# Optimization experiments

Measured on AMD Instinct MI355X. Metric: run time of the kernel, lower is better.

Reference implementation:

```python
import jax, jax.numpy as jnp
import numpy as np

# --- fan-beam (flat detector) FBP geometry constants, matching init geo dict ---
V, U = 720, 736            # sino_views, nDetecU
NX = NY = 512              # nVoxelX, nVoxelY
SVOX = 400.0               # sVoxelX = sVoxelY (mm)
DU = 1.2858                # dDetecU (mm)
DSO, DOD = 595.0, 490.6    # source-origin, origin-detector distances
DSD = DSO + DOD
DBETA = 2.0 * np.pi / V    # angular step (full 2*pi scan, endpoint=False)


def _ramp_filter_fft():
    """Ram-Lak ramp filter (Kak & Slaney discrete spatial kernel), FFT'd for fast conv."""
    n = np.arange(-(U - 1), U)
    h = np.zeros(2 * U - 1, np.float64)
    h[U - 1] = 1.0 / (4.0 * DU * DU)
    odd = (np.abs(n) % 2 == 1)
    h[odd] = -1.0 / (np.pi * n[odd] * DU) ** 2
    L = int(2 ** np.ceil(np.log2(2 * (2 * U - 1))))  # zero-pad length (linear conv)
    return jnp.asarray(np.fft.fft(h, L).astype(np.complex64)), L

_HF, _L = _ramp_filter_fft()


def setup_inputs() -> dict:
    key = jax.random.key(0)
    sinogram = jax.random.uniform(key, (1, 1, V, U), dtype=jnp.float32)
    return {"sinogram": sinogram}


def reference(sinogram):
    # --- 1) cosine weighting of each detector sample ---
    sino = sinogram.reshape(V, U)
    us = (jnp.arange(U, dtype=jnp.float32) - (U - 1) / 2.0) * DU  # detector coords
    sino_w = sino * (DSD / jnp.sqrt(DSD * DSD + us * us))

    # --- 2) Ram-Lak ramp filtering per view (FFT linear convolution) ---
    Qf = jnp.fft.ifft(jnp.fft.fft(sino_w, n=_L, axis=1) * _HF[None, :], axis=1)
    Q = (jnp.real(Qf)[:, U - 1:2 * U - 1] * DU).astype(jnp.float32)  # [V, U]

    # --- 3) weighted fan-beam backprojection (scan over angles, O(Nx*Ny) carry) ---
    dx = SVOX / NX
    xs = (jnp.arange(NX, dtype=jnp.float32) - (NX - 1) / 2.0) * dx
    X, Y = jnp.meshgrid(xs, xs, indexing='ij')  # [NX, NY]
    betas = jnp.linspace(0.0, 2.0 * np.pi, V, endpoint=False).astype(jnp.float32)

    def body(img, ang_q):
        beta, q = ang_q                       # q: filtered projection [U]
        cb, sb = jnp.cos(beta), jnp.sin(beta)
        t = X * cb + Y * sb                   # coord along detector direction
        s = -X * sb + Y * cb                  # coord toward source
        D = DSO - s                           # source-to-pixel axial distance
        u = DSD * t / D                       # flat-detector intersection (mm)
        idx = u / DU + (U - 1) / 2.0          # fractional detector index
        i0 = jnp.clip(jnp.floor(idx), 0, U - 2).astype(jnp.int32)
        f = idx - i0
        val = q[i0] * (1.0 - f) + q[i0 + 1] * f
        val = jnp.where((idx >= 0.0) & (idx <= U - 1.0), val, 0.0)
        return img + (DSO / D) ** 2 * val, None

    img0 = jnp.zeros((NX, NY), jnp.float32)
    img, _ = jax.lax.scan(body, img0, (betas, Q))
    # 0.5 factor: full 2*pi fan scan covers each ray twice
    return (img * (0.5 * DBETA)).reshape(1, 1, NX, NY)
```

## Files before the change

### kernel.cpp

```cpp
#include <hip/hip_runtime.h>
#include <math.h>

#define NV 720
#define NU 736
#define NUP 768
#define NXY 512
#define NM 368

__global__ __launch_bounds__(368) void prep_kernel(const float* __restrict__ sino,
                                                   float* __restrict__ swI,
                                                   float4* __restrict__ trig,
                                                   float* __restrict__ out_zero) {
    const int v = blockIdx.x;
    const int m = threadIdx.x;
    const int vb = v >> 2, vv = v & 3;
    const float DSD2 = (float)(1085.6 * 1085.6);
    #pragma unroll
    for (int pu = 0; pu < 2; ++pu) {
        const int u = 2 * m + pu;
        float us = ((float)u - 367.5f) * 1.2858f;
        float cw = 1085.6f / sqrtf(DSD2 + us * us);
        swI[((size_t)vb * NM + m) * 8 + pu * 4 + vv] = sino[v * NU + u] * cw;
    }
    if (m == 0) {
        float beta = (float)((double)v * (2.0 * M_PI / 720.0));
        float cb = cosf(beta), sb = sinf(beta);
        const float K = (float)(1085.6 / 1.2858);
        trig[v] = make_float4(cb * K, sb * K, cb, sb);
    }
    for (int i = v * 368 + m; i < NXY * NXY; i += 720 * 368)
        out_zero[i] = 0.0f;
}

__global__ __launch_bounds__(512) void filter_kernel(const float* __restrict__ swI,
                                                     float* __restrict__ Q) {
    __shared__ float wco[736];
    __shared__ float part[3][8][96];
    const int bx = blockIdx.x;
    const int q = bx & 3;
    const int vb = bx >> 2;
    const int v0 = vb * 4;
    const int tid = threadIdx.x;
    const int J0 = tid & 127;

    for (int i = tid; i < 736; i += 512) {
        double n = (double)(2 * i - 735);
        double a = M_PI * n * 1.2858;
        wco[i] = (float)(-1.0 / (a * a));
    }
    __syncthreads();

    const int m0 = __builtin_amdgcn_readfirstlane(92 * (tid >> 7));
    const int tz = m0 / 92;
    const float* sw = swI + (size_t)vb * NM * 8;
    const float* sp = sw + (size_t)m0 * 8;

    float a00 = 0.f, a01 = 0.f, a02 = 0.f, a03 = 0.f;
    float a10 = 0.f, a11 = 0.f, a12 = 0.f, a13 = 0.f;
    const int J0c = min(J0, 91);
    const int y0 = J0c + 367 + 92 * q;
    const float* wp = &wco[y0 - m0];

    #pragma unroll 4
    for (int mm = 0; mm < 92; ++mm) {
        const float w0 = wp[-mm];
        const float w1 = wp[1 - mm];
        const float* s = sp + mm * 8;
        const float s10 = s[4], s11 = s[5], s12 = s[6], s13 = s[7];
        const float s00 = s[0], s01 = s[1], s02 = s[2], s03 = s[3];
        a00 = fmaf(w0, s10, a00); a01 = fmaf(w0, s11, a01);
        a02 = fmaf(w0, s12, a02); a03 = fmaf(w0, s13, a03);
        a10 = fmaf(w1, s00, a10); a11 = fmaf(w1, s01, a11);
        a12 = fmaf(w1, s02, a12); a13 = fmaf(w1, s03, a13);
    }

    if (tz != 0 && J0 < 92) {
        part[tz - 1][0][J0] = a00; part[tz - 1][1][J0] = a01;
        part[tz - 1][2][J0] = a02; part[tz - 1][3][J0] = a03;
        part[tz - 1][4][J0] = a10; part[tz - 1][5][J0] = a11;
        part[tz - 1][6][J0] = a12; part[tz - 1][7][J0] = a13;
    }
    __syncthreads();

    if (tz == 0 && J0 < 92) {
        #pragma unroll
        for (int g = 0; g < 3; ++g) {
            a00 += part[g][0][J0]; a01 += part[g][1][J0];
            a02 += part[g][2][J0]; a03 += part[g][3][J0];
            a10 += part[g][4][J0]; a11 += part[g][5][J0];
            a12 += part[g][6][J0]; a13 += part[g][7][J0];
        }
        const float H0 = (float)(1.0 / (4.0 * 1.2858 * 1.2858));
        const int mc = J0 + 92 * q;
        const float4 c0 = *(const float4*)(sw + (size_t)mc * 8);
        const float4 c1 = *(const float4*)(sw + (size_t)mc * 8 + 4);
        a00 = fmaf(H0, c0.x, a00); a01 = fmaf(H0, c0.y, a01);
        a02 = fmaf(H0, c0.z, a02); a03 = fmaf(H0, c0.w, a03);
        a10 = fmaf(H0, c1.x, a10); a11 = fmaf(H0, c1.y, a11);
        a12 = fmaf(H0, c1.z, a12); a13 = fmaf(H0, c1.w, a13);
        const int j0i = 2 * (J0 + 92 * q);
        const float DU = 1.2858f;
        *(float2*)&Q[(v0 + 0) * NUP + j0i] = make_float2(a00 * DU, a10 * DU);
        *(float2*)&Q[(v0 + 1) * NUP + j0i] = make_float2(a01 * DU, a11 * DU);
        *(float2*)&Q[(v0 + 2) * NUP + j0i] = make_float2(a02 * DU, a12 * DU);
        *(float2*)&Q[(v0 + 3) * NUP + j0i] = make_float2(a03 * DU, a13 * DU);
    }
}

__global__ __launch_bounds__(256) void bp_kernel(const float* __restrict__ Q,
                                                 const float4* __restrict__ trig,
                                                 float* __restrict__ out) {
    __shared__ float win[2][4][NUP];
    const int b = blockIdx.x;
    const int c = b & 15;
    const int blk = b >> 4;
    const int bx = blk >> 4;
    const int by = blk & 15;
    const int t = threadIdx.x;
    const int w = t >> 6;
    const int l = t & 63;
    const int iq = (bx << 4) + ((w >> 1) << 3) + (l >> 3);
    const int jq = (by << 4) + ((w & 1) << 3) + (l & 7);

    const float dx = 400.0f / 512.0f;
    const float X = ((float)iq - 255.5f) * dx;
    const float Y = ((float)jq - 255.5f) * dx;
    const float Kc = (float)(1085.6 / 1.2858);

    float acc0 = 0.0f, acc1 = 0.0f, acc2 = 0.0f, acc3 = 0.0f;
    const bool inr = fmaf(X, X, Y * Y) <= 236.5f * 236.5f;
    const bool myint = __all(inr);

    const int nk = (c < 4) ? 12 : 11;
    const float* rowp = Q + (size_t)(c + 180 * w) * NUP;
    const float4* tvp = trig + c;

    #pragma unroll
    for (int ch = 0; ch < 3; ++ch)
        __builtin_amdgcn_global_load_lds(
            (const __attribute__((address_space(1))) void*)(rowp + ch * 256 + l * 4),
            (__attribute__((address_space(3))) void*)&win[0][w][ch * 256],
            16, 0, 0);

    for (int it = 0; it < nk; ++it) {
        __syncthreads();
        if (it + 1 < nk) {
            const float* rn = rowp + 16 * NUP;
            #pragma unroll
            for (int ch = 0; ch < 3; ++ch)
                __builtin_amdgcn_global_load_lds(
                    (const __attribute__((address_space(1))) void*)(rn + ch * 256 + l * 4),
                    (__attribute__((address_space(3))) void*)&win[(it + 1) & 1][w][ch * 256],
                    16, 0, 0);
        }
        const float* winf = &win[it & 1][0][0];

        if (myint) {
            const float4 tv = tvp[0];
            float a = fmaf(tv.z, X, tv.w * Y);
            float bb = fmaf(tv.z, Y, -tv.w * X);
            float aK = a * Kc, bK = bb * Kc;
            float D0 = 595.0f - bb, D1 = 595.0f + a, D2 = 595.0f + bb, D3 = 595.0f - a;
            float r0 = __builtin_amdgcn_rcpf(D0);
            float r1 = __builtin_amdgcn_rcpf(D1);
            float r2 = __builtin_amdgcn_rcpf(D2);
            float r3 = __builtin_amdgcn_rcpf(D3);
            float fi0 = fmaf(aK,  r0, 367.5f);
            float fi1 = fmaf(bK,  r1, 367.5f);
            float fi2 = fmaf(-aK, r2, 367.5f);
            float fi3 = fmaf(-bK, r3, 367.5f);
            int im[4] = {(int)fi0, (int)fi1, (int)fi2, (int)fi3};
            float ff[4] = {__builtin_amdgcn_fractf(fi0), __builtin_amdgcn_fractf(fi1),
                           __builtin_amdgcn_fractf(fi2), __builtin_amdgcn_fractf(fi3)};
            float gg[4] = {r0 * r0, r1 * r1, r2 * r2, r3 * r3};
            float* accp[4] = {&acc0, &acc1, &acc2, &acc3};
            #pragma unroll
            for (int m = 0; m < 4; ++m) {
                #pragma unroll
                for (int k = 0; k < 4; ++k) {
                    const float* p = winf + (k * NUP + im[m]);
                    float q0 = p[0];
                    float q1 = p[1];
                    float val = fmaf(ff[m], q1 - q0, q0);
                    *accp[(m - k) & 3] = fmaf(gg[m], val, *accp[(m - k) & 3]);
                }
            }
        } else {
            const float4 tvs[4] = {tvp[0], tvp[180], tvp[360], tvp[540]};
            const float pX[4] = {X, Y, -X, -Y};
            const float pY[4] = {Y, -X, -Y, X};
            float* accp[4] = {&acc0, &acc1, &acc2, &acc3};
            #pragma unroll
            for (int j = 0; j < 4; ++j) {
                float Xm = pX[j], Ym = pY[j];
                #pragma unroll
                for (int k = 0; k < 4; ++k) {
                    const float4 tv = tvs[k];
                    float t2 = fmaf(tv.x, Xm, tv.y * Ym);
                    float D  = fmaf(tv.w, Xm, fmaf(tv.z, -Ym, 595.0f));
                    float rD = __builtin_amdgcn_rcpf(D);
                    float fidx = fmaf(t2, rD, 367.5f);
                    int i0c = min(max((int)fidx, 0), NU - 2);
                    float f = __builtin_amdgcn_fractf(fidx);
                    const float* p = winf + (k * NUP + i0c);
                    float q0 = p[0];
                    float q1 = p[1];
                    float val = fmaf(f, q1 - q0, q0);
                    float cen = fidx - 367.5f;
                    float g = (__builtin_fabsf(cen) <= 367.5f) ? rD * rD : 0.0f;
                    *accp[j] = fmaf(g, val, *accp[j]);
                }
            }
        }
        rowp += 16 * NUP;
        tvp += 16;
    }
    const float SC = (float)(595.0 * 595.0 * 0.5 * (2.0 * M_PI / 720.0));
    const int ir = 511 - iq, jr = 511 - jq;
    unsafeAtomicAdd(&out[iq * NXY + jq], acc0 * SC);
    unsafeAtomicAdd(&out[jq * NXY + ir], acc1 * SC);
    unsafeAtomicAdd(&out[ir * NXY + jr], acc2 * SC);
    unsafeAtomicAdd(&out[jr * NXY + iq], acc3 * SC);
}

extern "C" void kernel_launch(void* const* d_in, const int* in_sizes, int n_in,
                              void* d_out, int out_size, void* d_ws, size_t ws_size,
                              hipStream_t stream) {
    const float* sino = (const float*)d_in[0];
    float* out = (float*)d_out;
    float* Q = (float*)d_ws;
    float4* trig = (float4*)((char*)d_ws + (size_t)NV * NUP * sizeof(float));
    float* swI = (float*)((char*)trig + (size_t)NV * sizeof(float4));

    prep_kernel<<<720, 368, 0, stream>>>(sino, swI, trig, out);
    filter_kernel<<<720, 512, 0, stream>>>(swI, Q);
    bp_kernel<<<4096, 256, 0, stream>>>(Q, trig, out);
}
```

Measured before the change: 117.5 us.

## Fuse prep, filter and backprojection into one persistent kernel with grid barriers

Replaces the three kernel launches with a single persistent kernel of 1024 blocks that synchronises phases through atomic-counter grid barriers. Cosine weighting now happens inside the filter phase in shared memory, so the swI intermediate and its global round trip go away. The backprojection phase loops over four pixel tiles per block instead of launching 4096 blocks. This removes launch gaps and one intermediate buffer, but adds a hipMemset launch and grid-barrier spin cost. It also assumes all 1024 blocks are co-resident; the barrier has a timeout that could silently break correctness if they are not.

```diff
diff --git a/kernel.cpp b/kernel.cpp
--- a/kernel.cpp
+++ b/kernel.cpp
@@ -5,222 +5,234 @@
 #define NU 736
 #define NUP 768
 #define NXY 512
-#define NM 368
-
-__global__ __launch_bounds__(368) void prep_kernel(const float* __restrict__ sino,
-                                                   float* __restrict__ swI,
-                                                   float4* __restrict__ trig,
-                                                   float* __restrict__ out_zero) {
-    const int v = blockIdx.x;
-    const int m = threadIdx.x;
-    const int vb = v >> 2, vv = v & 3;
-    const float DSD2 = (float)(1085.6 * 1085.6);
-    #pragma unroll
-    for (int pu = 0; pu < 2; ++pu) {
-        const int u = 2 * m + pu;
-        float us = ((float)u - 367.5f) * 1.2858f;
-        float cw = 1085.6f / sqrtf(DSD2 + us * us);
-        swI[((size_t)vb * NM + m) * 8 + pu * 4 + vv] = sino[v * NU + u] * cw;
-    }
-    if (m == 0) {
-        float beta = (float)((double)v * (2.0 * M_PI / 720.0));
+#define GRID 1024
+
+__device__ __forceinline__ void gsync(int* bar, int slot, int tid) {
+    __syncthreads();
+    if (tid == 0) {
+        __threadfence_system();
+        int* cnt = bar + 2 * slot;
+        int* flag = bar + 2 * slot + 1;
+        if (__hip_atomic_fetch_add(cnt, 1, __ATOMIC_ACQ_REL, __HIP_MEMORY_SCOPE_AGENT)
+            == GRID - 1) {
+            __hip_atomic_store(flag, 1, __ATOMIC_RELEASE, __HIP_MEMORY_SCOPE_AGENT);
+        } else {
+            long long t0 = clock64();
+            while (__hip_atomic_load(flag, __ATOMIC_ACQUIRE, __HIP_MEMORY_SCOPE_AGENT) == 0) {
+                __builtin_amdgcn_s_sleep(8);
+                if (clock64() - t0 > 100000000LL) break;
+            }
+        }
+        __threadfence_system();
+    }
+    __syncthreads();
+}
+
+__global__ __launch_bounds__(256, 4) void fused_kernel(const float* __restrict__ sino,
+                                                       float* __restrict__ Q,
+                                                       float4* __restrict__ trig,
+                                                       float* __restrict__ out,
+                                                       int* __restrict__ bar) {
+    __shared__ __align__(16) char smem[24576];
+    const int bid = blockIdx.x;
+    const int tid = threadIdx.x;
+    const int gid = bid * 256 + tid;
+
+    out[gid] = 0.0f;
+    if (gid < NV) {
+        float beta = (float)((double)gid * (2.0 * M_PI / 720.0));
         float cb = cosf(beta), sb = sinf(beta);
         const float K = (float)(1085.6 / 1.2858);
-        trig[v] = make_float4(cb * K, sb * K, cb, sb);
-    }
-    for (int i = v * 368 + m; i < NXY * NXY; i += 720 * 368)
-        out_zero[i] = 0.0f;
-}
-
-__global__ __launch_bounds__(512) void filter_kernel(const float* __restrict__ swI,
-                                                     float* __restrict__ Q) {
-    __shared__ float wco[736];
-    __shared__ float part[3][8][96];
-    const int bx = blockIdx.x;
-    const int q = bx & 3;
-    const int vb = bx >> 2;
-    const int v0 = vb * 4;
-    const int tid = threadIdx.x;
-    const int J0 = tid & 127;
-
-    for (int i = tid; i < 736; i += 512) {
-        double n = (double)(2 * i - 735);
-        double a = M_PI * n * 1.2858;
-        wco[i] = (float)(-1.0 / (a * a));
-    }
-    __syncthreads();
-
-    const int m0 = __builtin_amdgcn_readfirstlane(92 * (tid >> 7));
-    const int tz = m0 / 92;
-    const float* sw = swI + (size_t)vb * NM * 8;
-    const float* sp = sw + (size_t)m0 * 8;
-
-    float a00 = 0.f, a01 = 0.f, a02 = 0.f, a03 = 0.f;
-    float a10 = 0.f, a11 = 0.f, a12 = 0.f, a13 = 0.f;
-    const int J0c = min(J0, 91);
-    const int y0 = J0c + 367 + 92 * q;
-    const float* wp = &wco[y0 - m0];
-
-    #pragma unroll 4
-    for (int mm = 0; mm < 92; ++mm) {
-        const float w0 = wp[-mm];
-        const float w1 = wp[1 - mm];
-        const float* s = sp + mm * 8;
-        const float s10 = s[4], s11 = s[5], s12 = s[6], s13 = s[7];
-        const float s00 = s[0], s01 = s[1], s02 = s[2], s03 = s[3];
-        a00 = fmaf(w0, s10, a00); a01 = fmaf(w0, s11, a01);
-        a02 = fmaf(w0, s12, a02); a03 = fmaf(w0, s13, a03);
-        a10 = fmaf(w1, s00, a10); a11 = fmaf(w1, s01, a11);
-        a12 = fmaf(w1, s02, a12); a13 = fmaf(w1, s03, a13);
-    }
-
-    if (tz != 0 && J0 < 92) {
-        part[tz - 1][0][J0] = a00; part[tz - 1][1][J0] = a01;
-        part[tz - 1][2][J0] = a02; part[tz - 1][3][J0] = a03;
-        part[tz - 1][4][J0] = a10; part[tz - 1][5][J0] = a11;
-        part[tz - 1][6][J0] = a12; part[tz - 1][7][J0] = a13;
-    }
-    __syncthreads();
-
-    if (tz == 0 && J0 < 92) {
-        #pragma unroll
-        for (int g = 0; g < 3; ++g) {
-            a00 += part[g][0][J0]; a01 += part[g][1][J0];
-            a02 += part[g][2][J0]; a03 += part[g][3][J0];
-            a10 += part[g][4][J0]; a11 += part[g][5][J0];
-            a12 += part[g][6][J0]; a13 += part[g][7][J0];
-        }
-        const float H0 = (float)(1.0 / (4.0 * 1.2858 * 1.2858));
-        const int mc = J0 + 92 * q;
-        const float4 c0 = *(const float4*)(sw + (size_t)mc * 8);
-        const float4 c1 = *(const float4*)(sw + (size_t)mc * 8 + 4);
-        a00 = fmaf(H0, c0.x, a00); a01 = fmaf(H0, c0.y, a01);
-        a02 = fmaf(H0, c0.z, a02); a03 = fmaf(H0, c0.w, a03);
-        a10 = fmaf(H0, c1.x, a10); a11 = fmaf(H0, c1.y, a11);
-        a12 = fmaf(H0, c1.z, a12); a13 = fmaf(H0, c1.w, a13);
-        const int j0i = 2 * (J0 + 92 * q);
-        const float DU = 1.2858f;
-        *(float2*)&Q[(v0 + 0) * NUP + j0i] = make_float2(a00 * DU, a10 * DU);
-        *(float2*)&Q[(v0 + 1) * NUP + j0i] = make_float2(a01 * DU, a11 * DU);
-        *(float2*)&Q[(v0 + 2) * NUP + j0i] = make_float2(a02 * DU, a12 * DU);
-        *(float2*)&Q[(v0 + 3) * NUP + j0i] = make_float2(a03 * DU, a13 * DU);
-    }
-}
-
-__global__ __launch_bounds__(256) void bp_kernel(const float* __restrict__ Q,
-                                                 const float4* __restrict__ trig,
-                                                 float* __restrict__ out) {
-    __shared__ float win[2][4][NUP];
-    const int b = blockIdx.x;
-    const int c = b & 15;
-    const int blk = b >> 4;
-    const int bx = blk >> 4;
-    const int by = blk & 15;
-    const int t = threadIdx.x;
+        trig[gid] = make_float4(cb * K, sb * K, cb, sb);
+    }
+    gsync(bar, 0, tid);
+
+    if (bid < 720) {
+        float (*s4)[368][4] = (float(*)[368][4])smem;
+        float* wco = (float*)(smem + 11776);
+        float (*part)[96] = (float(*)[96])(smem + 14720);
+        const int q = bid & 3;
+        const int vb = bid >> 2;
+        const int v0 = vb * 4;
+        const int tz = tid >> 7;
+        const int J0 = tid & 127;
+
+        const float DSD2 = (float)(1085.6 * 1085.6);
+        for (int i = tid; i < 4 * NU; i += 256) {
+            const int vv = i / NU, u = i - vv * NU;
+            float us = ((float)u - 367.5f) * 1.2858f;
+            float cw = 1085.6f / sqrtf(DSD2 + us * us);
+            s4[u & 1][u >> 1][vv] = sino[(v0 + vv) * NU + u] * cw;
+        }
+        for (int i = tid; i < 736; i += 256) {
+            double n = (double)(2 * i - 735);
+            double a = M_PI * n * 1.2858;
+            wco[i] = (float)(-1.0 / (a * a));
+        }
+        __syncthreads();
+
+        const int m0 = 184 * tz;
+        float a00 = 0.f, a01 = 0.f, a02 = 0.f, a03 = 0.f;
+        float a10 = 0.f, a11 = 0.f, a12 = 0.f, a13 = 0.f;
+        const int J0c = min(J0, 91);
+        const int y0 = J0c + 367 + 92 * q;
+        const float* wp = &wco[y0 - m0];
+
+        #pragma unroll 4
+        for (int mm = 0; mm < 184; ++mm) {
+            const int m = m0 + mm;
+            const float w0 = wp[-mm];
+            const float w1 = wp[1 - mm];
+            const float4 sv1 = *(const float4*)&s4[1][m][0];
+            const float4 sv0 = *(const float4*)&s4[0][m][0];
+            a00 = fmaf(w0, sv1.x, a00); a01 = fmaf(w0, sv1.y, a01);
+            a02 = fmaf(w0, sv1.z, a02); a03 = fmaf(w0, sv1.w, a03);
+            a10 = fmaf(w1, sv0.x, a10); a11 = fmaf(w1, sv0.y, a11);
+            a12 = fmaf(w1, sv0.z, a12); a13 = fmaf(w1, sv0.w, a13);
+        }
+
+        if (tz == 1 && J0 < 92) {
+            part[0][J0] = a00; part[1][J0] = a01; part[2][J0] = a02; part[3][J0] = a03;
+            part[4][J0] = a10; part[5][J0] = a11; part[6][J0] = a12; part[7][J0] = a13;
+        }
+        __syncthreads();
+
+        if (tz == 0 && J0 < 92) {
+            a00 += part[0][J0]; a01 += part[1][J0];
+            a02 += part[2][J0]; a03 += part[3][J0];
+            a10 += part[4][J0]; a11 += part[5][J0];
+            a12 += part[6][J0]; a13 += part[7][J0];
+            const float H0 = (float)(1.0 / (4.0 * 1.2858 * 1.2858));
+            const int mc = J0 + 92 * q;
+            const float4 c0 = *(const float4*)&s4[0][mc][0];
+            const float4 c1 = *(const float4*)&s4[1][mc][0];
+            a00 = fmaf(H0, c0.x, a00); a01 = fmaf(H0, c0.y, a01);
+            a02 = fmaf(H0, c0.z, a02); a03 = fmaf(H0, c0.w, a03);
+            a10 = fmaf(H0, c1.x, a10); a11 = fmaf(H0, c1.y, a11);
+            a12 = fmaf(H0, c1.z, a12); a13 = fmaf(H0, c1.w, a13);
+            const int j0i = 2 * mc;
+            const float DU = 1.2858f;
+            *(float2*)&Q[(v0 + 0) * NUP + j0i] = make_float2(a00 * DU, a10 * DU);
+            *(float2*)&Q[(v0 + 1) * NUP + j0i] = make_float2(a01 * DU, a11 * DU);
+            *(float2*)&Q[(v0 + 2) * NUP + j0i] = make_float2(a02 * DU, a12 * DU);
+            *(float2*)&Q[(v0 + 3) * NUP + j0i] = make_float2(a03 * DU, a13 * DU);
+        }
+    }
+    gsync(bar, 1, tid);
+
+    float (*win)[4][NUP] = (float(*)[4][NUP])smem;
+    const int cc = bid & 15;
+    const int t = tid;
     const int w = t >> 6;
     const int l = t & 63;
-    const int iq = (bx << 4) + ((w >> 1) << 3) + (l >> 3);
-    const int jq = (by << 4) + ((w & 1) << 3) + (l & 7);
-
     const float dx = 400.0f / 512.0f;
-    const float X = ((float)iq - 255.5f) * dx;
-    const float Y = ((float)jq - 255.5f) * dx;
     const float Kc = (float)(1085.6 / 1.2858);
-
-    float acc0 = 0.0f, acc1 = 0.0f, acc2 = 0.0f, acc3 = 0.0f;
-    const bool inr = fmaf(X, X, Y * Y) <= 236.5f * 236.5f;
-    const bool myint = __all(inr);
-
-    const int nk = (c < 4) ? 12 : 11;
-    const float* rowp = Q + (size_t)(c + 180 * w) * NUP;
-    const float4* tvp = trig + c;
-
-    #pragma unroll
-    for (int ch = 0; ch < 3; ++ch)
-        __builtin_amdgcn_global_load_lds(
-            (const __attribute__((address_space(1))) void*)(rowp + ch * 256 + l * 4),
-            (__attribute__((address_space(3))) void*)&win[0][w][ch * 256],
-            16, 0, 0);
-
-    for (int it = 0; it < nk; ++it) {
+    const int nk = (cc < 4) ? 12 : 11;
+
+    #pragma unroll 1
+    for (int ti = 0; ti < 4; ++ti) {
+        const int blk = (bid >> 4) + ti * 64;
+        const int bx = blk >> 4;
+        const int by = blk & 15;
+        const int iq = (bx << 4) + ((w >> 1) << 3) + (l >> 3);
+        const int jq = (by << 4) + ((w & 1) << 3) + (l & 7);
+        const float X = ((float)iq - 255.5f) * dx;
+        const float Y = ((float)jq - 255.5f) * dx;
+        float acc0 = 0.0f, acc1 = 0.0f, acc2 = 0.0f, acc3 = 0.0f;
+        const bool inr = fmaf(X, X, Y * Y) <= 236.5f * 236.5f;
+        const bool myint = __all(inr);
+
+        const float* rowp = Q + (size_t)(cc + 180 * w) * NUP;
+        const float4* tvp = trig + cc;
+
         __syncthreads();
-        if (it + 1 < nk) {
-            const float* rn = rowp + 16 * NUP;
-            #pragma unroll
-            for (int ch = 0; ch < 3; ++ch)
-                __builtin_amdgcn_global_load_lds(
-                    (const __attribute__((address_space(1))) void*)(rn + ch * 256 + l * 4),
-                    (__attribute__((address_space(3))) void*)&win[(it + 1) & 1][w][ch * 256],
-                    16, 0, 0);
-        }
-        const float* winf = &win[it & 1][0][0];
-
-        if (myint) {
-            const float4 tv = tvp[0];
-            float a = fmaf(tv.z, X, tv.w * Y);
-            float bb = fmaf(tv.z, Y, -tv.w * X);
-            float aK = a * Kc, bK = bb * Kc;
-            float D0 = 595.0f - bb, D1 = 595.0f + a, D2 = 595.0f + bb, D3 = 595.0f - a;
-            float r0 = __builtin_amdgcn_rcpf(D0);
-            float r1 = __builtin_amdgcn_rcpf(D1);
-            float r2 = __builtin_amdgcn_rcpf(D2);
-            float r3 = __builtin_amdgcn_rcpf(D3);
-            float fi0 = fmaf(aK,  r0, 367.5f);
-            float fi1 = fmaf(bK,  r1, 367.5f);
-            float fi2 = fmaf(-aK, r2, 367.5f);
-            float fi3 = fmaf(-bK, r3, 367.5f);
-            int im[4] = {(int)fi0, (int)fi1, (int)fi2, (int)fi3};
-            float ff[4] = {__builtin_amdgcn_fractf(fi0), __builtin_amdgcn_fractf(fi1),
-                           __builtin_amdgcn_fractf(fi2), __builtin_amdgcn_fractf(fi3)};
-            float gg[4] = {r0 * r0, r1 * r1, r2 * r2, r3 * r3};
-            float* accp[4] = {&acc0, &acc1, &acc2, &acc3};
-            #pragma unroll
-            for (int m = 0; m < 4; ++m) {
+        #pragma unroll
+        for (int ch = 0; ch < 3; ++ch)
+            __builtin_amdgcn_global_load_lds(
+                (const __attribute__((address_space(1))) void*)(rowp + ch * 256 + l * 4),
+                (__attribute__((address_space(3))) void*)&win[0][w][ch * 256],
+                16, 0, 0);
+
+        for (int it = 0; it < nk; ++it) {
+            __syncthreads();
+            if (it + 1 < nk) {
+                const float* rn = rowp + 16 * NUP;
                 #pragma unroll
-                for (int k = 0; k < 4; ++k) {
-                    const float* p = winf + (k * NUP + im[m]);
-                    float q0 = p[0];
-                    float q1 = p[1];
-                    float val = fmaf(ff[m], q1 - q0, q0);
-                    *accp[(m - k) & 3] = fmaf(gg[m], val, *accp[(m - k) & 3]);
+                for (int ch = 0; ch < 3; ++ch)
+                    __builtin_amdgcn_global_load_lds(
+                        (const __attribute__((address_space(1))) void*)(rn + ch * 256 + l * 4),
+                        (__attribute__((address_space(3))) void*)&win[(it + 1) & 1][w][ch * 256],
+                        16, 0, 0);
+            }
+            const float* winf = &win[it & 1][0][0];
+
+            if (myint) {
+                const float4 tv = tvp[0];
+                float a = fmaf(tv.z, X, tv.w * Y);
+                float bb = fmaf(tv.z, Y, -tv.w * X);
+                float aK = a * Kc, bK = bb * Kc;
+                float D0 = 595.0f - bb, D1 = 595.0f + a, D2 = 595.0f + bb, D3 = 595.0f - a;
+                float r0 = __builtin_amdgcn_rcpf(D0);
+                float r1 = __builtin_amdgcn_rcpf(D1);
+                float r2 = __builtin_amdgcn_rcpf(D2);
+                float r3 = __builtin_amdgcn_rcpf(D3);
+                float fi0 = fmaf(aK,  r0, 367.5f);
+                float fi1 = fmaf(bK,  r1, 367.5f);
+                float fi2 = fmaf(-aK, r2, 367.5f);
+                float fi3 = fmaf(-bK, r3, 367.5f);
+                int im[4] = {(int)fi0, (int)fi1, (int)fi2, (int)fi3};
+                float ff[4] = {__builtin_amdgcn_fractf(fi0), __builtin_amdgcn_fractf(fi1),
+                               __builtin_amdgcn_fractf(fi2), __builtin_amdgcn_fractf(fi3)};
+                float gg[4] = {r0 * r0, r1 * r1, r2 * r2, r3 * r3};
+                float* accp[4] = {&acc0, &acc1, &acc2, &acc3};
+                #pragma unroll
+                for (int m = 0; m < 4; ++m) {
+                    #pragma unroll
+                    for (int k = 0; k < 4; ++k) {
+                        const float* p = winf + (k * NUP + im[m]);
+                        float q0 = p[0];
+                        float q1 = p[1];
+                        float val = fmaf(ff[m], q1 - q0, q0);
+                        *accp[(m - k) & 3] = fmaf(gg[m], val, *accp[(m - k) & 3]);
+                    }
+                }
+            } else {
+                const float4 tvs[4] = {tvp[0], tvp[180], tvp[360], tvp[540]};
+                const float pX[4] = {X, Y, -X, -Y};
+                const float pY[4] = {Y, -X, -Y, X};
+                float* accp[4] = {&acc0, &acc1, &acc2, &acc3};
+                #pragma unroll
+                for (int j = 0; j < 4; ++j) {
+                    float Xm = pX[j], Ym = pY[j];
+                    #pragma unroll
+                    for (int k = 0; k < 4; ++k) {
+                        const float4 tv = tvs[k];
+                        float t2 = fmaf(tv.x, Xm, tv.y * Ym);
+                        float D  = fmaf(tv.w, Xm, fmaf(tv.z, -Ym, 595.0f));
+                        float rD = __builtin_amdgcn_rcpf(D);
+                        float fidx = fmaf(t2, rD, 367.5f);
+                        int i0c = min(max((int)fidx, 0), NU - 2);
+                        float f = __builtin_amdgcn_fractf(fidx);
+                        const float* p = winf + (k * NUP + i0c);
+                        float q0 = p[0];
+                        float q1 = p[1];
+                        float val = fmaf(f, q1 - q0, q0);
+                        float cen = fidx - 367.5f;
+                        float g = (__builtin_fabsf(cen) <= 367.5f) ? rD * rD : 0.0f;
+                        *accp[j] = fmaf(g, val, *accp[j]);
+                    }
                 }
             }
-        } else {
-            const float4 tvs[4] = {tvp[0], tvp[180], tvp[360], tvp[540]};
-            const float pX[4] = {X, Y, -X, -Y};
-            const float pY[4] = {Y, -X, -Y, X};
-            float* accp[4] = {&acc0, &acc1, &acc2, &acc3};
-            #pragma unroll
-            for (int j = 0; j < 4; ++j) {
-                float Xm = pX[j], Ym = pY[j];
-                #pragma unroll
-                for (int k = 0; k < 4; ++k) {
-                    const float4 tv = tvs[k];
-                    float t2 = fmaf(tv.x, Xm, tv.y * Ym);
-                    float D  = fmaf(tv.w, Xm, fmaf(tv.z, -Ym, 595.0f));
-                    float rD = __builtin_amdgcn_rcpf(D);
-                    float fidx = fmaf(t2, rD, 367.5f);
-                    int i0c = min(max((int)fidx, 0), NU - 2);
-                    float f = __builtin_amdgcn_fractf(fidx);
-                    const float* p = winf + (k * NUP + i0c);
-                    float q0 = p[0];
-                    float q1 = p[1];
-                    float val = fmaf(f, q1 - q0, q0);
-                    float cen = fidx - 367.5f;
-                    float g = (__builtin_fabsf(cen) <= 367.5f) ? rD * rD : 0.0f;
-                    *accp[j] = fmaf(g, val, *accp[j]);
-                }
-            }
-        }
-        rowp += 16 * NUP;
-        tvp += 16;
-    }
-    const float SC = (float)(595.0 * 595.0 * 0.5 * (2.0 * M_PI / 720.0));
-    const int ir = 511 - iq, jr = 511 - jq;
-    unsafeAtomicAdd(&out[iq * NXY + jq], acc0 * SC);
-    unsafeAtomicAdd(&out[jq * NXY + ir], acc1 * SC);
-    unsafeAtomicAdd(&out[ir * NXY + jr], acc2 * SC);
-    unsafeAtomicAdd(&out[jr * NXY + iq], acc3 * SC);
+            rowp += 16 * NUP;
+            tvp += 16;
+        }
+        const float SC = (float)(595.0 * 595.0 * 0.5 * (2.0 * M_PI / 720.0));
+        const int ir = 511 - iq, jr = 511 - jq;
+        unsafeAtomicAdd(&out[iq * NXY + jq], acc0 * SC);
+        unsafeAtomicAdd(&out[jq * NXY + ir], acc1 * SC);
+        unsafeAtomicAdd(&out[ir * NXY + jr], acc2 * SC);
+        unsafeAtomicAdd(&out[jr * NXY + iq], acc3 * SC);
+    }
 }
 
 extern "C" void kernel_launch(void* const* d_in, const int* in_sizes, int n_in,
@@ -230,9 +242,8 @@
     float* out = (float*)d_out;
     float* Q = (float*)d_ws;
     float4* trig = (float4*)((char*)d_ws + (size_t)NV * NUP * sizeof(float));
-    float* swI = (float*)((char*)trig + (size_t)NV * sizeof(float4));
-
-    prep_kernel<<<720, 368, 0, stream>>>(sino, swI, trig, out);
-    filter_kernel<<<720, 512, 0, stream>>>(swI, Q);
-    bp_kernel<<<4096, 256, 0, stream>>>(Q, trig, out);
+    int* bar = (int*)((char*)trig + (size_t)NV * sizeof(float4));
+
+    hipMemsetAsync(bar, 0, 16, stream);
+    fused_kernel<<<GRID, 256, 0, stream>>>(sino, Q, trig, out, bar);
 }
```

Measured after the change: 351.9 us. 3x slower.

## Fuse cosine-weighting prep into filter kernel and raise backprojection wave priority

Applied to the files above, without the earlier changes.

Removes the separate prep kernel. Each filter block now cosine-weights its four views straight into an interleaved shared-memory buffer, and also zeroes the output and writes the trig table. This saves a kernel launch and a global round trip through the weighted-sinogram buffer. The cost is that each of the four blocks per view group recomputes the same weighting. Partial sums move to a float4-friendly layout, and s_setprio is raised around the backprojection compute section to favour compute waves over the loading phase.

```diff
diff --git a/kernel.cpp b/kernel.cpp
--- a/kernel.cpp
+++ b/kernel.cpp
@@ -5,44 +5,39 @@
 #define NU 736
 #define NUP 768
 #define NXY 512
-#define NM 368
-
-__global__ __launch_bounds__(368) void prep_kernel(const float* __restrict__ sino,
-                                                   float* __restrict__ swI,
-                                                   float4* __restrict__ trig,
-                                                   float* __restrict__ out_zero) {
-    const int v = blockIdx.x;
-    const int m = threadIdx.x;
-    const int vb = v >> 2, vv = v & 3;
-    const float DSD2 = (float)(1085.6 * 1085.6);
-    #pragma unroll
-    for (int pu = 0; pu < 2; ++pu) {
-        const int u = 2 * m + pu;
-        float us = ((float)u - 367.5f) * 1.2858f;
-        float cw = 1085.6f / sqrtf(DSD2 + us * us);
-        swI[((size_t)vb * NM + m) * 8 + pu * 4 + vv] = sino[v * NU + u] * cw;
-    }
-    if (m == 0) {
-        float beta = (float)((double)v * (2.0 * M_PI / 720.0));
-        float cb = cosf(beta), sb = sinf(beta);
-        const float K = (float)(1085.6 / 1.2858);
-        trig[v] = make_float4(cb * K, sb * K, cb, sb);
-    }
-    for (int i = v * 368 + m; i < NXY * NXY; i += 720 * 368)
-        out_zero[i] = 0.0f;
-}
-
-__global__ __launch_bounds__(512) void filter_kernel(const float* __restrict__ swI,
-                                                     float* __restrict__ Q) {
+
+__global__ __launch_bounds__(512) void filter_kernel(const float* __restrict__ sino,
+                                                     float* __restrict__ Q,
+                                                     float4* __restrict__ trig,
+                                                     float* __restrict__ out_zero) {
+    __shared__ float s4[2][368][4];
     __shared__ float wco[736];
-    __shared__ float part[3][8][96];
+    __shared__ float part[3][128][8];
     const int bx = blockIdx.x;
     const int q = bx & 3;
     const int vb = bx >> 2;
     const int v0 = vb * 4;
     const int tid = threadIdx.x;
+    const int tz = tid >> 7;
     const int J0 = tid & 127;
 
+    for (int i = bx * 512 + tid; i < NXY * NXY; i += 720 * 512)
+        out_zero[i] = 0.0f;
+
+    if (q == 0 && tid < 4) {
+        int v = v0 + tid;
+        float beta = (float)((double)v * (2.0 * M_PI / 720.0));
+        float cb = cosf(beta), sb = sinf(beta);
+        const float K = (float)(1085.6 / 1.2858);
+        trig[v] = make_float4(cb * K, sb * K, cb, sb);
+    }
+    const float DSD2 = (float)(1085.6 * 1085.6);
+    for (int i = tid; i < 4 * NU; i += 512) {
+        const int vv = i / NU, u = i - vv * NU;
+        float us = ((float)u - 367.5f) * 1.2858f;
+        float cw = 1085.6f / sqrtf(DSD2 + us * us);
+        s4[u & 1][u >> 1][vv] = sino[(v0 + vv) * NU + u] * cw;
+    }
     for (int i = tid; i < 736; i += 512) {
         double n = (double)(2 * i - 735);
         double a = M_PI * n * 1.2858;
@@ -50,11 +45,7 @@
     }
     __syncthreads();
 
-    const int m0 = __builtin_amdgcn_readfirstlane(92 * (tid >> 7));
-    const int tz = m0 / 92;
-    const float* sw = swI + (size_t)vb * NM * 8;
-    const float* sp = sw + (size_t)m0 * 8;
-
+    const int m0 = 92 * tz;
     float a00 = 0.f, a01 = 0.f, a02 = 0.f, a03 = 0.f;
     float a10 = 0.f, a11 = 0.f, a12 = 0.f, a13 = 0.f;
     const int J0c = min(J0, 91);
@@ -63,42 +54,40 @@
 
     #pragma unroll 4
     for (int mm = 0; mm < 92; ++mm) {
+        const int m = m0 + mm;
         const float w0 = wp[-mm];
         const float w1 = wp[1 - mm];
-        const float* s = sp + mm * 8;
-        const float s10 = s[4], s11 = s[5], s12 = s[6], s13 = s[7];
-        const float s00 = s[0], s01 = s[1], s02 = s[2], s03 = s[3];
-        a00 = fmaf(w0, s10, a00); a01 = fmaf(w0, s11, a01);
-        a02 = fmaf(w0, s12, a02); a03 = fmaf(w0, s13, a03);
-        a10 = fmaf(w1, s00, a10); a11 = fmaf(w1, s01, a11);
-        a12 = fmaf(w1, s02, a12); a13 = fmaf(w1, s03, a13);
+        const float4 sv1 = *(const float4*)&s4[1][m][0];
+        const float4 sv0 = *(const float4*)&s4[0][m][0];
+        a00 = fmaf(w0, sv1.x, a00); a01 = fmaf(w0, sv1.y, a01);
+        a02 = fmaf(w0, sv1.z, a02); a03 = fmaf(w0, sv1.w, a03);
+        a10 = fmaf(w1, sv0.x, a10); a11 = fmaf(w1, sv0.y, a11);
+        a12 = fmaf(w1, sv0.z, a12); a13 = fmaf(w1, sv0.w, a13);
     }
 
     if (tz != 0 && J0 < 92) {
-        part[tz - 1][0][J0] = a00; part[tz - 1][1][J0] = a01;
-        part[tz - 1][2][J0] = a02; part[tz - 1][3][J0] = a03;
-        part[tz - 1][4][J0] = a10; part[tz - 1][5][J0] = a11;
-        part[tz - 1][6][J0] = a12; part[tz - 1][7][J0] = a13;
+        *(float4*)&part[tz - 1][J0][0] = make_float4(a00, a01, a02, a03);
+        *(float4*)&part[tz - 1][J0][4] = make_float4(a10, a11, a12, a13);
     }
     __syncthreads();
 
     if (tz == 0 && J0 < 92) {
         #pragma unroll
         for (int g = 0; g < 3; ++g) {
-            a00 += part[g][0][J0]; a01 += part[g][1][J0];
-            a02 += part[g][2][J0]; a03 += part[g][3][J0];
-            a10 += part[g][4][J0]; a11 += part[g][5][J0];
-            a12 += part[g][6][J0]; a13 += part[g][7][J0];
+            const float4 p0 = *(const float4*)&part[g][J0][0];
+            const float4 p1 = *(const float4*)&part[g][J0][4];
+            a00 += p0.x; a01 += p0.y; a02 += p0.z; a03 += p0.w;
+            a10 += p1.x; a11 += p1.y; a12 += p1.z; a13 += p1.w;
         }
         const float H0 = (float)(1.0 / (4.0 * 1.2858 * 1.2858));
         const int mc = J0 + 92 * q;
-        const float4 c0 = *(const float4*)(sw + (size_t)mc * 8);
-        const float4 c1 = *(const float4*)(sw + (size_t)mc * 8 + 4);
+        const float4 c0 = *(const float4*)&s4[0][mc][0];
+        const float4 c1 = *(const float4*)&s4[1][mc][0];
         a00 = fmaf(H0, c0.x, a00); a01 = fmaf(H0, c0.y, a01);
         a02 = fmaf(H0, c0.z, a02); a03 = fmaf(H0, c0.w, a03);
         a10 = fmaf(H0, c1.x, a10); a11 = fmaf(H0, c1.y, a11);
         a12 = fmaf(H0, c1.z, a12); a13 = fmaf(H0, c1.w, a13);
-        const int j0i = 2 * (J0 + 92 * q);
+        const int j0i = 2 * mc;
         const float DU = 1.2858f;
         *(float2*)&Q[(v0 + 0) * NUP + j0i] = make_float2(a00 * DU, a10 * DU);
         *(float2*)&Q[(v0 + 1) * NUP + j0i] = make_float2(a01 * DU, a11 * DU);
@@ -155,6 +144,7 @@
         }
         const float* winf = &win[it & 1][0][0];
 
+        __builtin_amdgcn_s_setprio(1);
         if (myint) {
             const float4 tv = tvp[0];
             float a = fmaf(tv.z, X, tv.w * Y);
@@ -212,6 +202,7 @@
                 }
             }
         }
+        __builtin_amdgcn_s_setprio(0);
         rowp += 16 * NUP;
         tvp += 16;
     }
@@ -230,9 +221,7 @@
     float* out = (float*)d_out;
     float* Q = (float*)d_ws;
     float4* trig = (float4*)((char*)d_ws + (size_t)NV * NUP * sizeof(float));
-    float* swI = (float*)((char*)trig + (size_t)NV * sizeof(float4));
-
-    prep_kernel<<<720, 368, 0, stream>>>(sino, swI, trig, out);
-    filter_kernel<<<720, 512, 0, stream>>>(swI, Q);
+
+    filter_kernel<<<720, 512, 0, stream>>>(sino, Q, trig, out);
     bp_kernel<<<4096, 256, 0, stream>>>(Q, trig, out);
 }
```

Result: faster. 113.0 us (-3.9%).
